# Kernel tuning notes

Measured on AMD Instinct MI355X. Metric: run time of the kernel, lower is better.

Reference implementation:

```python
import jax, jax.numpy as jnp
import numpy as np

B, S, DIM = 2, 2048, 1024
HID = 2048          # multiple_of-rounded hidden dim
E, NSH, TOPK = 8, 2, 2


def _ffn(x, w1, w2, w3):
    return (jax.nn.silu(x @ w1.T) * (x @ w3.T)) @ w2.T


def setup_inputs() -> dict:
    key = jax.random.key(0)
    ks = jax.random.split(key, 8)
    sc = 0.02  # init scale for stability
    return {
        "x": jax.random.normal(ks[0], (B, S, DIM), jnp.float32),
        "router_w": jax.random.normal(ks[1], (E, DIM), jnp.float32) * sc,
        "expert_bias": jnp.zeros((E,), jnp.float32),
        "w1": jax.random.normal(ks[2], (E, HID, DIM), jnp.float32) * sc,
        "w3": jax.random.normal(ks[3], (E, HID, DIM), jnp.float32) * sc,
        "w2": jax.random.normal(ks[4], (E, DIM, HID), jnp.float32) * sc,
        "sw1": jax.random.normal(ks[5], (NSH, HID, DIM), jnp.float32) * sc,
        "sw3": jax.random.normal(ks[6], (NSH, HID, DIM), jnp.float32) * sc,
        "sw2": jax.random.normal(ks[7], (NSH, DIM, HID), jnp.float32) * sc,
    }


def reference(x, router_w, expert_bias, w1, w3, w2, sw1, sw3, sw2):
    bs, sl, d = x.shape
    xf = x.reshape(-1, d)  # [T, d]

    # shared experts (always-on)
    shared = jnp.zeros_like(xf)
    for i in range(sw1.shape[0]):
        shared = shared + _ffn(xf, sw1[i], sw2[i], sw3[i])

    # router with aux-free load-balance bias
    logits = xf @ router_w.T + expert_bias  # [T, E]
    rw, sel = jax.lax.top_k(logits, TOPK)   # [T, K]
    rw = jax.nn.softmax(rw.astype(jnp.float32), axis=-1).astype(x.dtype)

    # combine weights per (token, expert): sum of routing weights over topk slots
    onehot = jax.nn.one_hot(sel, E, dtype=x.dtype)        # [T, K, E]
    combine = jnp.einsum('tk,tke->te', rw, onehot)        # [T, E]

    # per-expert FFN accumulated via scan (equivalent to gather-FFN-scatter)
    def body(acc, ew):
        e1, e3, e2, cw = ew  # cw: [T]
        acc = acc + cw[:, None] * _ffn(xf, e1, e2, e3)
        return acc, None

    out, _ = jax.lax.scan(body, jnp.zeros_like(xf), (w1, w3, w2, combine.T))
    out = out + shared
    return out.reshape(bs, sl, -1)
```

## Files before the change

### kernel.cpp

```cpp
#include <hip/hip_runtime.h>
#include <stdint.h>

#define T_TOK 4096
#define DIMD  1024
#define HIDN  2048
#define NEXP  8
#define RMAX  9216
#define RROWS (RMAX + 2 * T_TOK)

typedef float f32x4 __attribute__((ext_vector_type(4)));
typedef short s16x8 __attribute__((ext_vector_type(8)));

__device__ __forceinline__ uint16_t f2bf(float f) {
    uint32_t u = __builtin_bit_cast(uint32_t, f);
    u += 0x7fffu + ((u >> 16) & 1u);
    return (uint16_t)(u >> 16);
}
__device__ __forceinline__ float bf2f(uint32_t h) {
    return __builtin_bit_cast(float, h << 16);
}
__device__ __forceinline__ uint32_t pk2(float a, float b) {
    return (uint32_t)f2bf(a) | ((uint32_t)f2bf(b) << 16);
}
__device__ __forceinline__ int swz(int r, int cbyte) {
    return r * 128 + (cbyte ^ ((r & 7) << 4));
}
__device__ __forceinline__ void gload16(const void* g, void* l) {
    __builtin_amdgcn_global_load_lds(
        (const __attribute__((address_space(1))) void*)g,
        (__attribute__((address_space(3))) void*)l, 16, 0, 0);
}
__device__ __forceinline__ void stage128x64(const uint16_t* gbase, int ldk,
                                            char* lds, int wv, int lane) {
    #pragma unroll
    for (int i = 0; i < 4; ++i) {
        int s = (wv * 4 + i) * 64 + lane;
        int row = s >> 3;
        int cb = ((s & 7) << 4) ^ ((row & 7) << 4);
        gload16(gbase + (size_t)row * ldk + (cb >> 1), lds + ((wv * 4 + i) << 10));
    }
}


struct CvtArgs {
    const float* s[7];
    uint16_t*    d[7];
    int          nq[7];
};

__global__ void cvt_all_kernel(CvtArgs a) {
    int base = blockIdx.x * blockDim.x + threadIdx.x;
    int stride = gridDim.x * blockDim.x;
    #pragma unroll
    for (int seg = 0; seg < 7; ++seg) {
        const float4* sp = (const float4*)a.s[seg];
        uint2* dp = (uint2*)a.d[seg];
        int n = a.nq[seg];
        for (int i = base; i < n; i += stride) {
            float4 v = sp[i];
            uint2 o; o.x = pk2(v.x, v.y); o.y = pk2(v.z, v.w);
            dp[i] = o;
        }
    }
}

__global__ __launch_bounds__(256)
void router_kernel(const float* __restrict__ x, const float* __restrict__ rw,
                   const float* __restrict__ bias,
                   int* __restrict__ sel, float* __restrict__ wgt,
                   int* __restrict__ cnt) {
    __shared__ float rws[NEXP * DIMD];
    int tid = threadIdx.x;
    for (int i = tid; i < NEXP * DIMD / 4; i += 256)
        ((float4*)rws)[i] = ((const float4*)rw)[i];
    __syncthreads();

    int wid = tid >> 6, lane = tid & 63;
    float b[NEXP];
    #pragma unroll
    for (int e = 0; e < NEXP; ++e) b[e] = bias[e];

    int t0 = (blockIdx.x * 4 + wid) * 8;
    for (int j = 0; j < 8; ++j) {
        int t = t0 + j;
        const float4* xr = (const float4*)(x + (size_t)t * DIMD);
        float p[NEXP] = {};
        #pragma unroll
        for (int c = 0; c < 4; ++c) {
            float4 xv = xr[c * 64 + lane];
            #pragma unroll
            for (int e = 0; e < NEXP; ++e) {
                float4 wv = *(const float4*)(rws + e * DIMD + c * 256 + lane * 4);
                p[e] += xv.x * wv.x + xv.y * wv.y + xv.z * wv.z + xv.w * wv.w;
            }
        }
        #pragma unroll
        for (int off = 32; off >= 1; off >>= 1) {
            #pragma unroll
            for (int e = 0; e < NEXP; ++e) p[e] += __shfl_xor(p[e], off, 64);
        }
        if (lane == 0) {
            #pragma unroll
            for (int e = 0; e < NEXP; ++e) p[e] += b[e];
            float l0 = -1e30f; int i0 = 0;
            #pragma unroll
            for (int e = 0; e < NEXP; ++e) { if (p[e] > l0) { l0 = p[e]; i0 = e; } }
            float l1 = -1e30f; int i1 = 0;
            #pragma unroll
            for (int e = 0; e < NEXP; ++e) { if (e == i0) continue; if (p[e] > l1) { l1 = p[e]; i1 = e; } }
            float e1 = expf(l1 - l0);
            float d = 1.f + e1;
            sel[t * 2] = i0; sel[t * 2 + 1] = i1;
            wgt[t * 2] = 1.f / d; wgt[t * 2 + 1] = e1 / d;
            atomicAdd(&cnt[i0], 1);
            atomicAdd(&cnt[i1], 1);
        }
    }
}

__global__ void offs_kernel(const int* __restrict__ cnt, int* __restrict__ offs) {
    if (threadIdx.x == 0 && blockIdx.x == 0) {
        int o = 0;
        for (int e = 0; e < NEXP; ++e) { offs[e] = o; o += (cnt[e] + 127) & ~127; }
        offs[NEXP] = o;
    }
}

__global__ void assign_kernel(const int* __restrict__ sel, const int* __restrict__ offs,
                              int* __restrict__ fill, int* __restrict__ row_of,
                              int* __restrict__ tok) {
    int i = blockIdx.x * blockDim.x + threadIdx.x;
    if (i < 2 * T_TOK) {
        int e = sel[i];
        int r = offs[e] + atomicAdd(&fill[e], 1);
        row_of[i] = r;
        tok[r] = i >> 1;
    } else if (i < 4 * T_TOK) {
        int j = i - 2 * T_TOK;
        tok[offs[NEXP] + j] = j & (T_TOK - 1);
    }
}

__global__ void combine_kernel(const uint16_t* __restrict__ H2, const int* __restrict__ row_of,
                               const float* __restrict__ wgt, const int* __restrict__ offs,
                               float* __restrict__ out) {
    int t = blockIdx.x;
    int c = threadIdx.x * 8;
    int r0 = row_of[t * 2], r1 = row_of[t * 2 + 1];
    int s0 = offs[NEXP] + t, s1 = s0 + T_TOK;
    float w0 = wgt[t * 2], w1 = wgt[t * 2 + 1];
    uint4 a = *(const uint4*)(H2 + (size_t)r0 * DIMD + c);
    uint4 b = *(const uint4*)(H2 + (size_t)r1 * DIMD + c);
    uint4 u = *(const uint4*)(H2 + (size_t)s0 * DIMD + c);
    uint4 v = *(const uint4*)(H2 + (size_t)s1 * DIMD + c);
    float4 o0, o1;
    o0.x = w0 * bf2f(a.x & 0xffffu) + w1 * bf2f(b.x & 0xffffu) + bf2f(u.x & 0xffffu) + bf2f(v.x & 0xffffu);
    o0.y = w0 * bf2f(a.x >> 16)     + w1 * bf2f(b.x >> 16)     + bf2f(u.x >> 16)     + bf2f(v.x >> 16);
    o0.z = w0 * bf2f(a.y & 0xffffu) + w1 * bf2f(b.y & 0xffffu) + bf2f(u.y & 0xffffu) + bf2f(v.y & 0xffffu);
    o0.w = w0 * bf2f(a.y >> 16)     + w1 * bf2f(b.y >> 16)     + bf2f(u.y >> 16)     + bf2f(v.y >> 16);
    o1.x = w0 * bf2f(a.z & 0xffffu) + w1 * bf2f(b.z & 0xffffu) + bf2f(u.z & 0xffffu) + bf2f(v.z & 0xffffu);
    o1.y = w0 * bf2f(a.z >> 16)     + w1 * bf2f(b.z >> 16)     + bf2f(u.z >> 16)     + bf2f(v.z >> 16);
    o1.z = w0 * bf2f(a.w & 0xffffu) + w1 * bf2f(b.w & 0xffffu) + bf2f(u.w & 0xffffu) + bf2f(v.w & 0xffffu);
    o1.w = w0 * bf2f(a.w >> 16)     + w1 * bf2f(b.w >> 16)     + bf2f(u.w >> 16)     + bf2f(v.w >> 16);
    float* o = out + (size_t)t * DIMD + c;
    *(float4*)o = o0;
    *(float4*)(o + 4) = o1;
}


__global__ __launch_bounds__(256, 2)
void gemm13_kernel(const uint16_t* __restrict__ xb, const int* __restrict__ tok,
                   const uint16_t* __restrict__ W1, const uint16_t* __restrict__ W3,
                   uint16_t* __restrict__ H, const int* __restrict__ offs) {
    __shared__ __align__(16) char lds[49152];
    char* As  = lds;
    char* B1s = lds + 16384;
    char* B3s = lds + 32768;

    const int K = DIMD;
    int row0 = blockIdx.y * 128;
    int rsh = row0 - offs[NEXP];
    int e;
    if (rsh >= 0) {
        if (rsh >= 2 * T_TOK) return;
        e = NEXP + (rsh >> 12);
    } else {
        e = 0;
        while (row0 >= offs[e + 1]) ++e;
    }
    const uint16_t* b1 = W1 + (size_t)e * HIDN * DIMD;
    const uint16_t* b3 = W3 + (size_t)e * HIDN * DIMD;
    int col0 = blockIdx.x * 128;

    int tid = threadIdx.x, lane = tid & 63;
    int wv = tid >> 6, wm = wv >> 1, wn = wv & 1;

    size_t abase[4];
    #pragma unroll
    for (int i = 0; i < 4; ++i) {
        int s = (wv * 4 + i) * 64 + lane;
        int row = s >> 3;
        int cb = ((s & 7) << 4) ^ ((row & 7) << 4);
        abase[i] = (size_t)tok[row0 + row] * DIMD + (cb >> 1);
    }

    f32x4 acc1[4][4] = {};
    f32x4 acc3[4][4] = {};

    for (int kt = 0; kt < K; kt += 64) {
        __syncthreads();
        #pragma unroll
        for (int i = 0; i < 4; ++i)
            gload16(xb + abase[i] + kt, As + ((wv * 4 + i) << 10));
        stage128x64(b1 + (size_t)col0 * K + kt, K, B1s, wv, lane);
        stage128x64(b3 + (size_t)col0 * K + kt, K, B3s, wv, lane);
        __syncthreads();

        #pragma unroll
        for (int s = 0; s < 2; ++s) {
            int cb = s * 64 + ((lane >> 4) << 4);
            s16x8 av[4];
            #pragma unroll
            for (int i = 0; i < 4; ++i)
                av[i] = *(const s16x8*)(As + swz(wm * 64 + i * 16 + (lane & 15), cb));
            #pragma unroll
            for (int j = 0; j < 4; ++j) {
                int br = wn * 64 + j * 16 + (lane & 15);
                s16x8 bv1 = *(const s16x8*)(B1s + swz(br, cb));
                s16x8 bv3 = *(const s16x8*)(B3s + swz(br, cb));
                #pragma unroll
                for (int i = 0; i < 4; ++i) {
                    acc1[i][j] = __builtin_amdgcn_mfma_f32_16x16x32_bf16(av[i], bv1, acc1[i][j], 0, 0, 0);
                    acc3[i][j] = __builtin_amdgcn_mfma_f32_16x16x32_bf16(av[i], bv3, acc3[i][j], 0, 0, 0);
                }
            }
        }
    }

    #pragma unroll
    for (int i = 0; i < 4; ++i) {
        #pragma unroll
        for (int j = 0; j < 4; ++j) {
            #pragma unroll
            for (int rg = 0; rg < 4; ++rg) {
                int row = row0 + wm * 64 + i * 16 + ((lane >> 4) << 2) + rg;
                int col = col0 + wn * 64 + j * 16 + (lane & 15);
                float a1 = acc1[i][j][rg];
                float a3 = acc3[i][j][rg];
                float hv = (a1 / (1.f + __expf(-a1))) * a3;
                H[(size_t)row * HIDN + col] = f2bf(hv);
            }
        }
    }
}

__global__ __launch_bounds__(256, 3)
void gemm2_kernel(const uint16_t* __restrict__ Hg,
                  const uint16_t* __restrict__ W2, uint16_t* __restrict__ H2,
                  const int* __restrict__ offs) {
    __shared__ __align__(16) char lds[32768];
    char* As = lds;
    char* Bs = lds + 16384;

    const int K = HIDN;
    int row0 = blockIdx.y * 128;
    int rsh = row0 - offs[NEXP];
    int e;
    if (rsh >= 0) {
        if (rsh >= 2 * T_TOK) return;
        e = NEXP + (rsh >> 12);
    } else {
        e = 0;
        while (row0 >= offs[e + 1]) ++e;
    }
    const uint16_t* b2 = W2 + (size_t)e * DIMD * HIDN;
    int col0 = blockIdx.x * 128;

    int tid = threadIdx.x, lane = tid & 63;
    int wv = tid >> 6, wm = wv >> 1, wn = wv & 1;

    f32x4 acc[4][4] = {};

    for (int kt = 0; kt < K; kt += 64) {
        __syncthreads();
        stage128x64(Hg + (size_t)row0 * K + kt, K, As, wv, lane);
        stage128x64(b2 + (size_t)col0 * K + kt, K, Bs, wv, lane);
        __syncthreads();

        #pragma unroll
        for (int s = 0; s < 2; ++s) {
            int cb = s * 64 + ((lane >> 4) << 4);
            s16x8 av[4];
            #pragma unroll
            for (int i = 0; i < 4; ++i)
                av[i] = *(const s16x8*)(As + swz(wm * 64 + i * 16 + (lane & 15), cb));
            #pragma unroll
            for (int j = 0; j < 4; ++j) {
                s16x8 bv = *(const s16x8*)(Bs + swz(wn * 64 + j * 16 + (lane & 15), cb));
                #pragma unroll
                for (int i = 0; i < 4; ++i)
                    acc[i][j] = __builtin_amdgcn_mfma_f32_16x16x32_bf16(av[i], bv, acc[i][j], 0, 0, 0);
            }
        }
    }

    #pragma unroll
    for (int i = 0; i < 4; ++i) {
        #pragma unroll
        for (int j = 0; j < 4; ++j) {
            #pragma unroll
            for (int rg = 0; rg < 4; ++rg) {
                int row = row0 + wm * 64 + i * 16 + ((lane >> 4) << 2) + rg;
                int col = col0 + wn * 64 + j * 16 + (lane & 15);
                H2[(size_t)row * DIMD + col] = f2bf(acc[i][j][rg]);
            }
        }
    }
}


extern "C" void kernel_launch(void* const* d_in, const int* in_sizes, int n_in,
                              void* d_out, int out_size, void* d_ws, size_t ws_size,
                              hipStream_t stream) {
    const float* x   = (const float*)d_in[0];
    const float* rw  = (const float*)d_in[1];
    const float* eb  = (const float*)d_in[2];
    const float* w1  = (const float*)d_in[3];
    const float* w3  = (const float*)d_in[4];
    const float* w2  = (const float*)d_in[5];
    const float* sw1 = (const float*)d_in[6];
    const float* sw3 = (const float*)d_in[7];
    const float* sw2 = (const float*)d_in[8];
    float* out = (float*)d_out;

    const int EW = NEXP * HIDN * DIMD;
    const int SW = 2 * HIDN * DIMD;

    char* ws = (char*)d_ws;
    size_t off = 0;
    auto alloc = [&](size_t b) { char* p = ws + off; off = (off + b + 255) & ~(size_t)255; return p; };
    uint16_t* xb    = (uint16_t*)alloc((size_t)T_TOK * DIMD * 2);
    uint16_t* Hg    = (uint16_t*)alloc((size_t)RROWS * HIDN * 2);
    uint16_t* H2    = (uint16_t*)alloc((size_t)RROWS * DIMD * 2);
    uint16_t* w1all = (uint16_t*)alloc((size_t)(EW + SW) * 2);
    uint16_t* w3all = (uint16_t*)alloc((size_t)(EW + SW) * 2);
    uint16_t* w2all = (uint16_t*)alloc((size_t)(EW + SW) * 2);
    int*   sel    = (int*)  alloc(T_TOK * 2 * 4);
    float* wgt    = (float*)alloc(T_TOK * 2 * 4);
    int*   row_of = (int*)  alloc(T_TOK * 2 * 4);
    int*   tok    = (int*)  alloc(RROWS * 4);
    int*   cnt    = (int*)  alloc(64);
    int*   fill   = (int*)  alloc(64);
    int*   offs   = (int*)  alloc(64);

    hipMemsetAsync(cnt, 0, 64, stream);
    hipMemsetAsync(fill, 0, 64, stream);
    hipMemsetAsync(tok, 0, RROWS * 4, stream);

    CvtArgs ca;
    ca.s[0] = w1;  ca.d[0] = w1all;      ca.nq[0] = EW / 4;
    ca.s[1] = sw1; ca.d[1] = w1all + EW; ca.nq[1] = SW / 4;
    ca.s[2] = w3;  ca.d[2] = w3all;      ca.nq[2] = EW / 4;
    ca.s[3] = sw3; ca.d[3] = w3all + EW; ca.nq[3] = SW / 4;
    ca.s[4] = w2;  ca.d[4] = w2all;      ca.nq[4] = EW / 4;
    ca.s[5] = sw2; ca.d[5] = w2all + EW; ca.nq[5] = SW / 4;
    ca.s[6] = x;   ca.d[6] = xb;         ca.nq[6] = T_TOK * DIMD / 4;
    cvt_all_kernel<<<2048, 256, 0, stream>>>(ca);

    router_kernel<<<128, 256, 0, stream>>>(x, rw, eb, sel, wgt, cnt);
    offs_kernel<<<1, 1, 0, stream>>>(cnt, offs);
    assign_kernel<<<64, 256, 0, stream>>>(sel, offs, fill, row_of, tok);

    gemm13_kernel<<<dim3(HIDN / 128, RROWS / 128), 256, 0, stream>>>(xb, tok, w1all, w3all, Hg, offs);
    gemm2_kernel<<<dim3(DIMD / 128, RROWS / 128), 256, 0, stream>>>(Hg, w2all, H2, offs);

    combine_kernel<<<T_TOK, 128, 0, stream>>>(H2, row_of, wgt, offs, out);
}
```

Baseline: 473.5 us.

## Interleave W1/W3 weights and use triple-buffered 256-row 8-wave GEMM kernel

Weight conversion now interleaves W1 and W3 rows in 16-row groups, so one GEMM over N=4096 computes both projections and applies SiLU-gating in the epilogue. The two GEMM kernels are replaced by a single templated kernel with 512 threads, 256x128 tiles, a 3-stage LDS ring fed by direct global-to-LDS loads, manual waitcnt/barrier scheduling and raised MFMA priority. Expert row padding grows to 256, which pads more rows and needs a larger RMAX. The aim is to hide global load latency and raise MFMA utilisation. The cost is heavy LDS use (144KB) and more wasted padded work.

```diff
diff --git a/kernel.cpp b/kernel.cpp
--- a/kernel.cpp
+++ b/kernel.cpp
@@ -5,7 +5,7 @@
 #define DIMD  1024
 #define HIDN  2048
 #define NEXP  8
-#define RMAX  9216
+#define RMAX  10240
 #define RROWS (RMAX + 2 * T_TOK)
 
 typedef float f32x4 __attribute__((ext_vector_type(4)));
@@ -30,22 +30,16 @@
         (const __attribute__((address_space(1))) void*)g,
         (__attribute__((address_space(3))) void*)l, 16, 0, 0);
 }
-__device__ __forceinline__ void stage128x64(const uint16_t* gbase, int ldk,
-                                            char* lds, int wv, int lane) {
-    #pragma unroll
-    for (int i = 0; i < 4; ++i) {
-        int s = (wv * 4 + i) * 64 + lane;
-        int row = s >> 3;
-        int cb = ((s & 7) << 4) ^ ((row & 7) << 4);
-        gload16(gbase + (size_t)row * ldk + (cb >> 1), lds + ((wv * 4 + i) << 10));
-    }
-}
+#define BAR()      asm volatile("s_barrier" ::: "memory")
+#define WAIT_VM(n) asm volatile("s_waitcnt vmcnt(" #n ")" ::: "memory")
+#define WAIT_LGKM0() asm volatile("s_waitcnt lgkmcnt(0)" ::: "memory")
 
 
 struct CvtArgs {
     const float* s[7];
     uint16_t*    d[7];
     int          nq[7];
+    int          mode[7];
 };
 
 __global__ void cvt_all_kernel(CvtArgs a) {
@@ -56,10 +50,20 @@
         const float4* sp = (const float4*)a.s[seg];
         uint2* dp = (uint2*)a.d[seg];
         int n = a.nq[seg];
+        int mode = a.mode[seg];
         for (int i = base; i < n; i += stride) {
             float4 v = sp[i];
             uint2 o; o.x = pk2(v.x, v.y); o.y = pk2(v.z, v.w);
-            dp[i] = o;
+            int di = i;
+            if (mode) {
+                int e = i >> 19;
+                int rem = i & 524287;
+                int nr = rem >> 8;
+                int kq = rem & 255;
+                int np = ((nr >> 4) << 5) + ((mode == 2) ? 16 : 0) + (nr & 15);
+                di = (e << 20) + (np << 8) + kq;
+            }
+            dp[di] = o;
         }
     }
 }
@@ -121,7 +125,7 @@
 __global__ void offs_kernel(const int* __restrict__ cnt, int* __restrict__ offs) {
     if (threadIdx.x == 0 && blockIdx.x == 0) {
         int o = 0;
-        for (int e = 0; e < NEXP; ++e) { offs[e] = o; o += (cnt[e] + 127) & ~127; }
+        for (int e = 0; e < NEXP; ++e) { offs[e] = o; o += (cnt[e] + 255) & ~255; }
         offs[NEXP] = o;
     }
 }
@@ -167,18 +171,14 @@
     *(float4*)(o + 4) = o1;
 }
 
-
-__global__ __launch_bounds__(256, 2)
-void gemm13_kernel(const uint16_t* __restrict__ xb, const int* __restrict__ tok,
-                   const uint16_t* __restrict__ W1, const uint16_t* __restrict__ W3,
-                   uint16_t* __restrict__ H, const int* __restrict__ offs) {
-    __shared__ __align__(16) char lds[49152];
-    char* As  = lds;
-    char* B1s = lds + 16384;
-    char* B3s = lds + 32768;
-
-    const int K = DIMD;
-    int row0 = blockIdx.y * 128;
+template<int IND, int SILU>
+__global__ __launch_bounds__(512, 2)
+void gemm8p_kernel(const uint16_t* __restrict__ A, const int* __restrict__ tok,
+                   const uint16_t* __restrict__ W, uint16_t* __restrict__ Cout,
+                   const int* __restrict__ offs, int N, int K) {
+    __shared__ __align__(16) char lds[3 * 49152];
+
+    int row0 = blockIdx.y * 256;
     int rsh = row0 - offs[NEXP];
     int e;
     if (rsh >= 0) {
@@ -188,131 +188,131 @@
         e = 0;
         while (row0 >= offs[e + 1]) ++e;
     }
-    const uint16_t* b1 = W1 + (size_t)e * HIDN * DIMD;
-    const uint16_t* b3 = W3 + (size_t)e * HIDN * DIMD;
+    const uint16_t* wp = W + (size_t)e * ((size_t)N * K);
     int col0 = blockIdx.x * 128;
 
     int tid = threadIdx.x, lane = tid & 63;
-    int wv = tid >> 6, wm = wv >> 1, wn = wv & 1;
-
-    size_t abase[4];
+    int wid = tid >> 6, wm = wid >> 1, wn = wid & 1;
+
+    uint32_t asrc[4];
+    #pragma unroll
+    for (int p = 0; p < 4; ++p) {
+        int s = p * 512 + tid;
+        int r = s >> 3;
+        int cb = ((s & 7) << 4) ^ ((r & 7) << 4);
+        int grow = IND ? tok[row0 + r] : (row0 + r);
+        asrc[p] = (uint32_t)grow * (uint32_t)K + (cb >> 1);
+    }
+    uint32_t bsrc[2];
+    #pragma unroll
+    for (int p = 0; p < 2; ++p) {
+        int s = p * 512 + tid;
+        int r = s >> 3;
+        int cb = ((s & 7) << 4) ^ ((r & 7) << 4);
+        bsrc[p] = (uint32_t)(col0 + r) * (uint32_t)K + (cb >> 1);
+    }
+    int ldsA = wid * 1024;
+    int ldsB = 32768 + wid * 1024;
+
+    int nt = K / 64;
+    f32x4 acc[4][4] = {};
+
+    auto STAGE = [&](int t) {
+        char* buf = lds + (t % 3) * 49152;
+        int kt = t * 64;
+        #pragma unroll
+        for (int p = 0; p < 4; ++p)
+            gload16(A + asrc[p] + kt, buf + p * 8192 + ldsA);
+        #pragma unroll
+        for (int p = 0; p < 2; ++p)
+            gload16(wp + bsrc[p] + kt, buf + 32768 + p * 8192 + (ldsB - 32768));
+    };
+
+    int arow = wm * 64 + (lane & 15);
+    int brow = wn * 64 + (lane & 15);
+    int khi = (lane >> 4) << 4;
+
+    STAGE(0);
+    STAGE(1);
+    WAIT_VM(6);
+    BAR();
+
+    for (int t = 0; t < nt; ++t) {
+        char* As = lds + (t % 3) * 49152;
+        char* Bs = As + 32768;
+
+        s16x8 av[2][4], bv[2][2];
+        #pragma unroll
+        for (int ks = 0; ks < 2; ++ks)
+            #pragma unroll
+            for (int i = 0; i < 4; ++i)
+                av[ks][i] = *(const s16x8*)(As + swz(arow + i * 16, ks * 64 + khi));
+        #pragma unroll
+        for (int ks = 0; ks < 2; ++ks)
+            #pragma unroll
+            for (int j = 0; j < 2; ++j)
+                bv[ks][j] = *(const s16x8*)(Bs + swz(brow + j * 16, ks * 64 + khi));
+        if (t + 2 < nt) STAGE(t + 2);
+        BAR();
+        WAIT_LGKM0();
+        __builtin_amdgcn_s_setprio(1);
+        #pragma unroll
+        for (int ks = 0; ks < 2; ++ks)
+            #pragma unroll
+            for (int j = 0; j < 2; ++j)
+                #pragma unroll
+                for (int i = 0; i < 4; ++i)
+                    acc[i][j] = __builtin_amdgcn_mfma_f32_16x16x32_bf16(av[ks][i], bv[ks][j], acc[i][j], 0, 0, 0);
+        __builtin_amdgcn_s_setprio(0);
+        BAR();
+
+        s16x8 bv2[2][2];
+        #pragma unroll
+        for (int ks = 0; ks < 2; ++ks)
+            #pragma unroll
+            for (int j = 0; j < 2; ++j)
+                bv2[ks][j] = *(const s16x8*)(Bs + swz(brow + (j + 2) * 16, ks * 64 + khi));
+        BAR();
+        WAIT_LGKM0();
+        __builtin_amdgcn_s_setprio(1);
+        #pragma unroll
+        for (int ks = 0; ks < 2; ++ks)
+            #pragma unroll
+            for (int j = 0; j < 2; ++j)
+                #pragma unroll
+                for (int i = 0; i < 4; ++i)
+                    acc[i][j + 2] = __builtin_amdgcn_mfma_f32_16x16x32_bf16(av[ks][i], bv2[ks][j], acc[i][j + 2], 0, 0, 0);
+        __builtin_amdgcn_s_setprio(0);
+        if (t + 2 < nt) {
+            WAIT_VM(6);
+        } else if (t + 1 < nt) {
+            WAIT_VM(0);
+        }
+        BAR();
+    }
+
     #pragma unroll
     for (int i = 0; i < 4; ++i) {
-        int s = (wv * 4 + i) * 64 + lane;
-        int row = s >> 3;
-        int cb = ((s & 7) << 4) ^ ((row & 7) << 4);
-        abase[i] = (size_t)tok[row0 + row] * DIMD + (cb >> 1);
-    }
-
-    f32x4 acc1[4][4] = {};
-    f32x4 acc3[4][4] = {};
-
-    for (int kt = 0; kt < K; kt += 64) {
-        __syncthreads();
-        #pragma unroll
-        for (int i = 0; i < 4; ++i)
-            gload16(xb + abase[i] + kt, As + ((wv * 4 + i) << 10));
-        stage128x64(b1 + (size_t)col0 * K + kt, K, B1s, wv, lane);
-        stage128x64(b3 + (size_t)col0 * K + kt, K, B3s, wv, lane);
-        __syncthreads();
-
-        #pragma unroll
-        for (int s = 0; s < 2; ++s) {
-            int cb = s * 64 + ((lane >> 4) << 4);
-            s16x8 av[4];
-            #pragma unroll
-            for (int i = 0; i < 4; ++i)
-                av[i] = *(const s16x8*)(As + swz(wm * 64 + i * 16 + (lane & 15), cb));
-            #pragma unroll
-            for (int j = 0; j < 4; ++j) {
-                int br = wn * 64 + j * 16 + (lane & 15);
-                s16x8 bv1 = *(const s16x8*)(B1s + swz(br, cb));
-                s16x8 bv3 = *(const s16x8*)(B3s + swz(br, cb));
+        int row = row0 + wm * 64 + i * 16 + ((lane >> 4) << 2);
+        if (SILU) {
+            #pragma unroll
+            for (int m = 0; m < 2; ++m) {
+                int hc = ((col0 + wn * 64) >> 1) + m * 16 + (lane & 15);
                 #pragma unroll
-                for (int i = 0; i < 4; ++i) {
-                    acc1[i][j] = __builtin_amdgcn_mfma_f32_16x16x32_bf16(av[i], bv1, acc1[i][j], 0, 0, 0);
-                    acc3[i][j] = __builtin_amdgcn_mfma_f32_16x16x32_bf16(av[i], bv3, acc3[i][j], 0, 0, 0);
+                for (int rg = 0; rg < 4; ++rg) {
+                    float a1 = acc[i][2 * m][rg];
+                    float a3 = acc[i][2 * m + 1][rg];
+                    float hv = (a1 / (1.f + __expf(-a1))) * a3;
+                    Cout[(size_t)(row + rg) * HIDN + hc] = f2bf(hv);
                 }
             }
-        }
-    }
-
-    #pragma unroll
-    for (int i = 0; i < 4; ++i) {
-        #pragma unroll
-        for (int j = 0; j < 4; ++j) {
-            #pragma unroll
-            for (int rg = 0; rg < 4; ++rg) {
-                int row = row0 + wm * 64 + i * 16 + ((lane >> 4) << 2) + rg;
-                int col = col0 + wn * 64 + j * 16 + (lane & 15);
-                float a1 = acc1[i][j][rg];
-                float a3 = acc3[i][j][rg];
-                float hv = (a1 / (1.f + __expf(-a1))) * a3;
-                H[(size_t)row * HIDN + col] = f2bf(hv);
-            }
-        }
-    }
-}
-
-__global__ __launch_bounds__(256, 3)
-void gemm2_kernel(const uint16_t* __restrict__ Hg,
-                  const uint16_t* __restrict__ W2, uint16_t* __restrict__ H2,
-                  const int* __restrict__ offs) {
-    __shared__ __align__(16) char lds[32768];
-    char* As = lds;
-    char* Bs = lds + 16384;
-
-    const int K = HIDN;
-    int row0 = blockIdx.y * 128;
-    int rsh = row0 - offs[NEXP];
-    int e;
-    if (rsh >= 0) {
-        if (rsh >= 2 * T_TOK) return;
-        e = NEXP + (rsh >> 12);
-    } else {
-        e = 0;
-        while (row0 >= offs[e + 1]) ++e;
-    }
-    const uint16_t* b2 = W2 + (size_t)e * DIMD * HIDN;
-    int col0 = blockIdx.x * 128;
-
-    int tid = threadIdx.x, lane = tid & 63;
-    int wv = tid >> 6, wm = wv >> 1, wn = wv & 1;
-
-    f32x4 acc[4][4] = {};
-
-    for (int kt = 0; kt < K; kt += 64) {
-        __syncthreads();
-        stage128x64(Hg + (size_t)row0 * K + kt, K, As, wv, lane);
-        stage128x64(b2 + (size_t)col0 * K + kt, K, Bs, wv, lane);
-        __syncthreads();
-
-        #pragma unroll
-        for (int s = 0; s < 2; ++s) {
-            int cb = s * 64 + ((lane >> 4) << 4);
-            s16x8 av[4];
-            #pragma unroll
-            for (int i = 0; i < 4; ++i)
-                av[i] = *(const s16x8*)(As + swz(wm * 64 + i * 16 + (lane & 15), cb));
+        } else {
             #pragma unroll
             for (int j = 0; j < 4; ++j) {
-                s16x8 bv = *(const s16x8*)(Bs + swz(wn * 64 + j * 16 + (lane & 15), cb));
+                int c = col0 + wn * 64 + j * 16 + (lane & 15);
                 #pragma unroll
-                for (int i = 0; i < 4; ++i)
-                    acc[i][j] = __builtin_amdgcn_mfma_f32_16x16x32_bf16(av[i], bv, acc[i][j], 0, 0, 0);
-            }
-        }
-    }
-
-    #pragma unroll
-    for (int i = 0; i < 4; ++i) {
-        #pragma unroll
-        for (int j = 0; j < 4; ++j) {
-            #pragma unroll
-            for (int rg = 0; rg < 4; ++rg) {
-                int row = row0 + wm * 64 + i * 16 + ((lane >> 4) << 2) + rg;
-                int col = col0 + wn * 64 + j * 16 + (lane & 15);
-                H2[(size_t)row * DIMD + col] = f2bf(acc[i][j][rg]);
+                for (int rg = 0; rg < 4; ++rg)
+                    Cout[(size_t)(row + rg) * N + c] = f2bf(acc[i][j][rg]);
             }
         }
     }
@@ -333,8 +333,8 @@
     const float* sw2 = (const float*)d_in[8];
     float* out = (float*)d_out;
 
-    const int EW = NEXP * HIDN * DIMD;
-    const int SW = 2 * HIDN * DIMD;
+    const size_t EW = (size_t)NEXP * HIDN * DIMD;
+    const size_t SW = (size_t)2 * HIDN * DIMD;
 
     char* ws = (char*)d_ws;
     size_t off = 0;
@@ -342,9 +342,8 @@
     uint16_t* xb    = (uint16_t*)alloc((size_t)T_TOK * DIMD * 2);
     uint16_t* Hg    = (uint16_t*)alloc((size_t)RROWS * HIDN * 2);
     uint16_t* H2    = (uint16_t*)alloc((size_t)RROWS * DIMD * 2);
-    uint16_t* w1all = (uint16_t*)alloc((size_t)(EW + SW) * 2);
-    uint16_t* w3all = (uint16_t*)alloc((size_t)(EW + SW) * 2);
-    uint16_t* w2all = (uint16_t*)alloc((size_t)(EW + SW) * 2);
+    uint16_t* w13   = (uint16_t*)alloc((size_t)10 * 4096 * 1024 * 2);
+    uint16_t* w2all = (uint16_t*)alloc((EW + SW) * 2);
     int*   sel    = (int*)  alloc(T_TOK * 2 * 4);
     float* wgt    = (float*)alloc(T_TOK * 2 * 4);
     int*   row_of = (int*)  alloc(T_TOK * 2 * 4);
@@ -358,21 +357,21 @@
     hipMemsetAsync(tok, 0, RROWS * 4, stream);
 
     CvtArgs ca;
-    ca.s[0] = w1;  ca.d[0] = w1all;      ca.nq[0] = EW / 4;
-    ca.s[1] = sw1; ca.d[1] = w1all + EW; ca.nq[1] = SW / 4;
-    ca.s[2] = w3;  ca.d[2] = w3all;      ca.nq[2] = EW / 4;
-    ca.s[3] = sw3; ca.d[3] = w3all + EW; ca.nq[3] = SW / 4;
-    ca.s[4] = w2;  ca.d[4] = w2all;      ca.nq[4] = EW / 4;
-    ca.s[5] = sw2; ca.d[5] = w2all + EW; ca.nq[5] = SW / 4;
-    ca.s[6] = x;   ca.d[6] = xb;         ca.nq[6] = T_TOK * DIMD / 4;
+    ca.s[0] = w1;  ca.d[0] = w13;                          ca.nq[0] = (int)(EW / 4); ca.mode[0] = 1;
+    ca.s[1] = sw1; ca.d[1] = w13 + (size_t)8 * 4096 * 1024; ca.nq[1] = (int)(SW / 4); ca.mode[1] = 1;
+    ca.s[2] = w3;  ca.d[2] = w13;                          ca.nq[2] = (int)(EW / 4); ca.mode[2] = 2;
+    ca.s[3] = sw3; ca.d[3] = w13 + (size_t)8 * 4096 * 1024; ca.nq[3] = (int)(SW / 4); ca.mode[3] = 2;
+    ca.s[4] = w2;  ca.d[4] = w2all;                        ca.nq[4] = (int)(EW / 4); ca.mode[4] = 0;
+    ca.s[5] = sw2; ca.d[5] = w2all + EW;                   ca.nq[5] = (int)(SW / 4); ca.mode[5] = 0;
+    ca.s[6] = x;   ca.d[6] = xb;                           ca.nq[6] = T_TOK * DIMD / 4; ca.mode[6] = 0;
     cvt_all_kernel<<<2048, 256, 0, stream>>>(ca);
 
     router_kernel<<<128, 256, 0, stream>>>(x, rw, eb, sel, wgt, cnt);
     offs_kernel<<<1, 1, 0, stream>>>(cnt, offs);
     assign_kernel<<<64, 256, 0, stream>>>(sel, offs, fill, row_of, tok);
 
-    gemm13_kernel<<<dim3(HIDN / 128, RROWS / 128), 256, 0, stream>>>(xb, tok, w1all, w3all, Hg, offs);
-    gemm2_kernel<<<dim3(DIMD / 128, RROWS / 128), 256, 0, stream>>>(Hg, w2all, H2, offs);
+    gemm8p_kernel<1, 1><<<dim3(32, RROWS / 256), 512, 0, stream>>>(xb, tok, w13, Hg, offs, 4096, 1024);
+    gemm8p_kernel<0, 0><<<dim3(8, RROWS / 256), 512, 0, stream>>>(Hg, nullptr, w2all, H2, offs, 1024, 2048);
 
     combine_kernel<<<T_TOK, 128, 0, stream>>>(H2, row_of, wgt, offs, out);
 }
```

After: 521.2 us. +10.1%, slower.

## Interleave W1/W3 weights and use 256x256 double-buffered 8-wave gemm13 pipeline

Applied to the files above, without the earlier changes.

Weights w1 and w3 are converted into one interleaved [E, 4096, 1024] bf16 matrix, in alternating 16-row groups, so a single GEMM produces gate and up columns side by side. The gemm13 kernel becomes a 512-thread, 256x256-tile kernel with double-buffered 128KB LDS. It prefetches the next k-tile in stages alongside MFMA phases, using manual barriers, waitcnt and setprio. Expert row padding grows to 256 (RMAX raised to match) to fit the larger tile, which adds padding work, and the large LDS footprint limits occupancy.

```diff
diff --git a/kernel.cpp b/kernel.cpp
--- a/kernel.cpp
+++ b/kernel.cpp
@@ -5,7 +5,7 @@
 #define DIMD  1024
 #define HIDN  2048
 #define NEXP  8
-#define RMAX  9216
+#define RMAX  10240
 #define RROWS (RMAX + 2 * T_TOK)
 
 typedef float f32x4 __attribute__((ext_vector_type(4)));
@@ -30,6 +30,11 @@
         (const __attribute__((address_space(1))) void*)g,
         (__attribute__((address_space(3))) void*)l, 16, 0, 0);
 }
+#define BAR()        asm volatile("s_barrier" ::: "memory")
+#define WAIT_VM4()   asm volatile("s_waitcnt vmcnt(4)" ::: "memory")
+#define WAIT_VM0()   asm volatile("s_waitcnt vmcnt(0)" ::: "memory")
+#define WAIT_LGKM0() asm volatile("s_waitcnt lgkmcnt(0)" ::: "memory")
+
 __device__ __forceinline__ void stage128x64(const uint16_t* gbase, int ldk,
                                             char* lds, int wv, int lane) {
     #pragma unroll
@@ -46,6 +51,7 @@
     const float* s[7];
     uint16_t*    d[7];
     int          nq[7];
+    int          mode[7];
 };
 
 __global__ void cvt_all_kernel(CvtArgs a) {
@@ -56,10 +62,20 @@
         const float4* sp = (const float4*)a.s[seg];
         uint2* dp = (uint2*)a.d[seg];
         int n = a.nq[seg];
+        int mode = a.mode[seg];
         for (int i = base; i < n; i += stride) {
             float4 v = sp[i];
             uint2 o; o.x = pk2(v.x, v.y); o.y = pk2(v.z, v.w);
-            dp[i] = o;
+            int di = i;
+            if (mode) {
+                int e = i >> 19;
+                int rem = i & 524287;
+                int nr = rem >> 8;
+                int kq = rem & 255;
+                int np = ((nr >> 4) << 5) + ((mode == 2) ? 16 : 0) + (nr & 15);
+                di = (e << 20) + (np << 8) + kq;
+            }
+            dp[di] = o;
         }
     }
 }
@@ -121,7 +137,7 @@
 __global__ void offs_kernel(const int* __restrict__ cnt, int* __restrict__ offs) {
     if (threadIdx.x == 0 && blockIdx.x == 0) {
         int o = 0;
-        for (int e = 0; e < NEXP; ++e) { offs[e] = o; o += (cnt[e] + 127) & ~127; }
+        for (int e = 0; e < NEXP; ++e) { offs[e] = o; o += (cnt[e] + 255) & ~255; }
         offs[NEXP] = o;
     }
 }
@@ -167,18 +183,15 @@
     *(float4*)(o + 4) = o1;
 }
 
-
-__global__ __launch_bounds__(256, 2)
-void gemm13_kernel(const uint16_t* __restrict__ xb, const int* __restrict__ tok,
-                   const uint16_t* __restrict__ W1, const uint16_t* __restrict__ W3,
-                   uint16_t* __restrict__ H, const int* __restrict__ offs) {
-    __shared__ __align__(16) char lds[49152];
-    char* As  = lds;
-    char* B1s = lds + 16384;
-    char* B3s = lds + 32768;
-
-    const int K = DIMD;
-    int row0 = blockIdx.y * 128;
+__global__ __launch_bounds__(512, 2)
+void gemm13_8p(const uint16_t* __restrict__ A, const int* __restrict__ tok,
+               const uint16_t* __restrict__ W, uint16_t* __restrict__ H,
+               const int* __restrict__ offs) {
+    constexpr int K = DIMD;
+    constexpr int NT = K / 64;
+    __shared__ __align__(16) char lds[131072];
+
+    int row0 = blockIdx.y * 256;
     int rsh = row0 - offs[NEXP];
     int e;
     if (rsh >= 0) {
@@ -188,67 +201,121 @@
         e = 0;
         while (row0 >= offs[e + 1]) ++e;
     }
-    const uint16_t* b1 = W1 + (size_t)e * HIDN * DIMD;
-    const uint16_t* b3 = W3 + (size_t)e * HIDN * DIMD;
-    int col0 = blockIdx.x * 128;
-
-    int tid = threadIdx.x, lane = tid & 63;
-    int wv = tid >> 6, wm = wv >> 1, wn = wv & 1;
-
-    size_t abase[4];
-    #pragma unroll
-    for (int i = 0; i < 4; ++i) {
-        int s = (wv * 4 + i) * 64 + lane;
-        int row = s >> 3;
-        int cb = ((s & 7) << 4) ^ ((row & 7) << 4);
-        abase[i] = (size_t)tok[row0 + row] * DIMD + (cb >> 1);
-    }
-
-    f32x4 acc1[4][4] = {};
-    f32x4 acc3[4][4] = {};
-
-    for (int kt = 0; kt < K; kt += 64) {
-        __syncthreads();
-        #pragma unroll
-        for (int i = 0; i < 4; ++i)
-            gload16(xb + abase[i] + kt, As + ((wv * 4 + i) << 10));
-        stage128x64(b1 + (size_t)col0 * K + kt, K, B1s, wv, lane);
-        stage128x64(b3 + (size_t)col0 * K + kt, K, B3s, wv, lane);
-        __syncthreads();
-
-        #pragma unroll
-        for (int s = 0; s < 2; ++s) {
-            int cb = s * 64 + ((lane >> 4) << 4);
-            s16x8 av[4];
+    const uint16_t* wp = W + (size_t)e * (4096ull * 1024ull);
+    int col0 = blockIdx.x * 256;
+
+    int tid = threadIdx.x, lane = tid & 63, wid = tid >> 6;
+    int wm = wid >> 2, wn = wid & 3;
+
+    int sslot = (lane & 3) ^ ((lane >> 2) & 3);
+    uint32_t aoff[2], boff[2];
+    #pragma unroll
+    for (int i = 0; i < 2; ++i) {
+        int r = i * 128 + (tid >> 2);
+        int garow = tok[row0 + r];
+        aoff[i] = (uint32_t)garow * K + sslot * 8;
+        boff[i] = (uint32_t)(col0 + r) * K + sslot * 8;
+    }
+    int ldsw = wid * 1024;
+
+    int rslot = ((lane >> 4) ^ (lane & 3)) << 4;
+    int aro = (wm * 128 + (lane & 15)) * 64 + rslot;
+    int bro = (wn * 64 + (lane & 15)) * 64 + rslot;
+
+    #define STAGE_A(buf, kt, ks) { \
+        gload16(A + aoff[0] + (kt) + (ks) * 32, (buf) + (ks) * 16384 + ldsw); \
+        gload16(A + aoff[1] + (kt) + (ks) * 32, (buf) + (ks) * 16384 + 8192 + ldsw); }
+    #define STAGE_B(buf, kt, ks) { \
+        gload16(wp + boff[0] + (kt) + (ks) * 32, (buf) + 32768 + (ks) * 16384 + ldsw); \
+        gload16(wp + boff[1] + (kt) + (ks) * 32, (buf) + 32768 + (ks) * 16384 + 8192 + ldsw); }
+
+    STAGE_A(lds, 0, 0); STAGE_B(lds, 0, 0);
+    STAGE_A(lds, 0, 1); STAGE_B(lds, 0, 1);
+    WAIT_VM4();
+    BAR();
+
+    f32x4 acc[8][4] = {};
+
+    for (int t = 0; t < NT; ++t) {
+        char* cur = lds + (t & 1) * 65536;
+        char* nxt = lds + ((t + 1) & 1) * 65536;
+        int kt1 = (t + 1) * 64;
+        bool pre = (t + 1 < NT);
+        s16x8 av[4], bv[4], av2[4];
+
+        #pragma unroll
+        for (int f = 0; f < 4; ++f) av[f] = *(const s16x8*)(cur + aro + f * 1024);
+        #pragma unroll
+        for (int f = 0; f < 4; ++f) bv[f] = *(const s16x8*)(cur + 32768 + bro + f * 1024);
+        if (pre) STAGE_A(nxt, kt1, 0);
+        BAR(); WAIT_LGKM0();
+        __builtin_amdgcn_s_setprio(1);
+        #pragma unroll
+        for (int j = 0; j < 4; ++j)
             #pragma unroll
             for (int i = 0; i < 4; ++i)
-                av[i] = *(const s16x8*)(As + swz(wm * 64 + i * 16 + (lane & 15), cb));
-            #pragma unroll
-            for (int j = 0; j < 4; ++j) {
-                int br = wn * 64 + j * 16 + (lane & 15);
-                s16x8 bv1 = *(const s16x8*)(B1s + swz(br, cb));
-                s16x8 bv3 = *(const s16x8*)(B3s + swz(br, cb));
-                #pragma unroll
-                for (int i = 0; i < 4; ++i) {
-                    acc1[i][j] = __builtin_amdgcn_mfma_f32_16x16x32_bf16(av[i], bv1, acc1[i][j], 0, 0, 0);
-                    acc3[i][j] = __builtin_amdgcn_mfma_f32_16x16x32_bf16(av[i], bv3, acc3[i][j], 0, 0, 0);
-                }
-            }
-        }
-    }
-
-    #pragma unroll
-    for (int i = 0; i < 4; ++i) {
-        #pragma unroll
-        for (int j = 0; j < 4; ++j) {
+                acc[i][j] = __builtin_amdgcn_mfma_f32_16x16x32_bf16(av[i], bv[j], acc[i][j], 0, 0, 0);
+        __builtin_amdgcn_s_setprio(0);
+        BAR();
+
+        #pragma unroll
+        for (int f = 0; f < 4; ++f) av2[f] = *(const s16x8*)(cur + aro + (f + 4) * 1024);
+        if (pre) STAGE_B(nxt, kt1, 0);
+        BAR(); WAIT_LGKM0();
+        __builtin_amdgcn_s_setprio(1);
+        #pragma unroll
+        for (int j = 0; j < 4; ++j)
+            #pragma unroll
+            for (int i = 0; i < 4; ++i)
+                acc[i + 4][j] = __builtin_amdgcn_mfma_f32_16x16x32_bf16(av2[i], bv[j], acc[i + 4][j], 0, 0, 0);
+        __builtin_amdgcn_s_setprio(0);
+        if (pre) { WAIT_VM4(); } else { WAIT_VM0(); }
+        BAR();
+
+        #pragma unroll
+        for (int f = 0; f < 4; ++f) av[f] = *(const s16x8*)(cur + 16384 + aro + f * 1024);
+        #pragma unroll
+        for (int f = 0; f < 4; ++f) bv[f] = *(const s16x8*)(cur + 32768 + 16384 + bro + f * 1024);
+        if (pre) STAGE_A(nxt, kt1, 1);
+        BAR(); WAIT_LGKM0();
+        __builtin_amdgcn_s_setprio(1);
+        #pragma unroll
+        for (int j = 0; j < 4; ++j)
+            #pragma unroll
+            for (int i = 0; i < 4; ++i)
+                acc[i][j] = __builtin_amdgcn_mfma_f32_16x16x32_bf16(av[i], bv[j], acc[i][j], 0, 0, 0);
+        __builtin_amdgcn_s_setprio(0);
+        BAR();
+
+        #pragma unroll
+        for (int f = 0; f < 4; ++f) av2[f] = *(const s16x8*)(cur + 16384 + aro + (f + 4) * 1024);
+        if (pre) STAGE_B(nxt, kt1, 1);
+        BAR(); WAIT_LGKM0();
+        __builtin_amdgcn_s_setprio(1);
+        #pragma unroll
+        for (int j = 0; j < 4; ++j)
+            #pragma unroll
+            for (int i = 0; i < 4; ++i)
+                acc[i + 4][j] = __builtin_amdgcn_mfma_f32_16x16x32_bf16(av2[i], bv[j], acc[i + 4][j], 0, 0, 0);
+        __builtin_amdgcn_s_setprio(0);
+        if (pre) WAIT_VM4();
+        BAR();
+    }
+    #undef STAGE_A
+    #undef STAGE_B
+
+    #pragma unroll
+    for (int i = 0; i < 8; ++i) {
+        int row = row0 + wm * 128 + i * 16 + ((lane >> 4) << 2);
+        #pragma unroll
+        for (int m = 0; m < 2; ++m) {
+            int hc = ((col0 + wn * 64) >> 1) + m * 16 + (lane & 15);
             #pragma unroll
             for (int rg = 0; rg < 4; ++rg) {
-                int row = row0 + wm * 64 + i * 16 + ((lane >> 4) << 2) + rg;
-                int col = col0 + wn * 64 + j * 16 + (lane & 15);
-                float a1 = acc1[i][j][rg];
-                float a3 = acc3[i][j][rg];
+                float a1 = acc[i][2 * m][rg];
+                float a3 = acc[i][2 * m + 1][rg];
                 float hv = (a1 / (1.f + __expf(-a1))) * a3;
-                H[(size_t)row * HIDN + col] = f2bf(hv);
+                H[(size_t)(row + rg) * HIDN + hc] = f2bf(hv);
             }
         }
     }
@@ -333,8 +400,8 @@
     const float* sw2 = (const float*)d_in[8];
     float* out = (float*)d_out;
 
-    const int EW = NEXP * HIDN * DIMD;
-    const int SW = 2 * HIDN * DIMD;
+    const size_t EW = (size_t)NEXP * HIDN * DIMD;
+    const size_t SW = (size_t)2 * HIDN * DIMD;
 
     char* ws = (char*)d_ws;
     size_t off = 0;
@@ -342,9 +409,8 @@
     uint16_t* xb    = (uint16_t*)alloc((size_t)T_TOK * DIMD * 2);
     uint16_t* Hg    = (uint16_t*)alloc((size_t)RROWS * HIDN * 2);
     uint16_t* H2    = (uint16_t*)alloc((size_t)RROWS * DIMD * 2);
-    uint16_t* w1all = (uint16_t*)alloc((size_t)(EW + SW) * 2);
-    uint16_t* w3all = (uint16_t*)alloc((size_t)(EW + SW) * 2);
-    uint16_t* w2all = (uint16_t*)alloc((size_t)(EW + SW) * 2);
+    uint16_t* w13   = (uint16_t*)alloc((size_t)10 * 4096 * 1024 * 2);
+    uint16_t* w2all = (uint16_t*)alloc((EW + SW) * 2);
     int*   sel    = (int*)  alloc(T_TOK * 2 * 4);
     float* wgt    = (float*)alloc(T_TOK * 2 * 4);
     int*   row_of = (int*)  alloc(T_TOK * 2 * 4);
@@ -358,20 +424,20 @@
     hipMemsetAsync(tok, 0, RROWS * 4, stream);
 
     CvtArgs ca;
-    ca.s[0] = w1;  ca.d[0] = w1all;      ca.nq[0] = EW / 4;
-    ca.s[1] = sw1; ca.d[1] = w1all + EW; ca.nq[1] = SW / 4;
-    ca.s[2] = w3;  ca.d[2] = w3all;      ca.nq[2] = EW / 4;
-    ca.s[3] = sw3; ca.d[3] = w3all + EW; ca.nq[3] = SW / 4;
-    ca.s[4] = w2;  ca.d[4] = w2all;      ca.nq[4] = EW / 4;
-    ca.s[5] = sw2; ca.d[5] = w2all + EW; ca.nq[5] = SW / 4;
-    ca.s[6] = x;   ca.d[6] = xb;         ca.nq[6] = T_TOK * DIMD / 4;
+    ca.s[0] = w1;  ca.d[0] = w13;                           ca.nq[0] = (int)(EW / 4); ca.mode[0] = 1;
+    ca.s[1] = sw1; ca.d[1] = w13 + (size_t)8 * 4096 * 1024; ca.nq[1] = (int)(SW / 4); ca.mode[1] = 1;
+    ca.s[2] = w3;  ca.d[2] = w13;                           ca.nq[2] = (int)(EW / 4); ca.mode[2] = 2;
+    ca.s[3] = sw3; ca.d[3] = w13 + (size_t)8 * 4096 * 1024; ca.nq[3] = (int)(SW / 4); ca.mode[3] = 2;
+    ca.s[4] = w2;  ca.d[4] = w2all;                         ca.nq[4] = (int)(EW / 4); ca.mode[4] = 0;
+    ca.s[5] = sw2; ca.d[5] = w2all + EW;                    ca.nq[5] = (int)(SW / 4); ca.mode[5] = 0;
+    ca.s[6] = x;   ca.d[6] = xb;                            ca.nq[6] = T_TOK * DIMD / 4; ca.mode[6] = 0;
     cvt_all_kernel<<<2048, 256, 0, stream>>>(ca);
 
     router_kernel<<<128, 256, 0, stream>>>(x, rw, eb, sel, wgt, cnt);
     offs_kernel<<<1, 1, 0, stream>>>(cnt, offs);
     assign_kernel<<<64, 256, 0, stream>>>(sel, offs, fill, row_of, tok);
 
-    gemm13_kernel<<<dim3(HIDN / 128, RROWS / 128), 256, 0, stream>>>(xb, tok, w1all, w3all, Hg, offs);
+    gemm13_8p<<<dim3(16, RROWS / 256), 512, 0, stream>>>(xb, tok, w13, Hg, offs);
     gemm2_kernel<<<dim3(DIMD / 128, RROWS / 128), 256, 0, stream>>>(Hg, w2all, H2, offs);
 
     combine_kernel<<<T_TOK, 128, 0, stream>>>(H2, row_of, wgt, offs, out);
```

Measured after the change: 492.4 us. 1.04x slower.
